# Performance work log

Hardware: AMD Instinct MI355X
Metric: run time of the kernel (lower is better)

Reference implementation:

```python
import jax, jax.numpy as jnp
import numpy as np

L = 2      # decoder layers
B = 4      # batch
T = 1000   # seq_len (mask built for this length)
C = 768    # input_dim / d_model
H = 12     # num_heads
DK = C // H
WIN = 100


def layernorm(x, g, b):
    m = x.mean(-1, keepdims=True)
    v = x.var(-1, keepdims=True)
    return (x - m) / jnp.sqrt(v + 1e-5) * g + b


def pos_encoding(t, c):
    # Transformer-XL / espnet RelPositionalEncoding table: relative positions t-1 .. -(t-1)
    rel = jnp.arange(t - 1, -t, -1, dtype=jnp.float32)          # (2t-1,)
    div = jnp.exp(-jnp.arange(0, c, 2, dtype=jnp.float32) * (np.log(10000.0) / c))
    ang = rel[:, None] * div[None, :]                            # (2t-1, c/2)
    pe = jnp.zeros((2 * t - 1, c), dtype=jnp.float32)
    pe = pe.at[:, 0::2].set(jnp.sin(ang)).at[:, 1::2].set(jnp.cos(ang))
    return pe


def rel_shift(x):
    # x: (B, H, T, 2T-1) -> (B, H, T, T), Transformer-XL relative shift
    b, h, t, p = x.shape
    xp = jnp.pad(x, ((0, 0), (0, 0), (0, 0), (1, 0)))
    xp = xp.reshape(b, h, p + 1, t)[:, :, 1:, :].reshape(b, h, t, p)
    return xp[..., :t]


def setup_inputs() -> dict:
    key = jax.random.key(0)
    ks = jax.random.split(key, 16)
    s = 0.02
    inp = {
        "x": jax.random.normal(ks[0], (B, T, C), dtype=jnp.float32),
        "Wq": jax.random.normal(ks[1], (L, C, C), dtype=jnp.float32) * s,
        "bq": jnp.zeros((L, C), dtype=jnp.float32),
        "Wk": jax.random.normal(ks[2], (L, C, C), dtype=jnp.float32) * s,
        "bk": jnp.zeros((L, C), dtype=jnp.float32),
        "Wv": jax.random.normal(ks[3], (L, C, C), dtype=jnp.float32) * s,
        "bv": jnp.zeros((L, C), dtype=jnp.float32),
        "Wo": jax.random.normal(ks[4], (L, C, C), dtype=jnp.float32) * s,
        "bo": jnp.zeros((L, C), dtype=jnp.float32),
        "Wp": jax.random.normal(ks[5], (L, C, C), dtype=jnp.float32) * s,   # linear_pos, no bias
        "pos_u": jax.random.normal(ks[6], (L, H, DK), dtype=jnp.float32) * s,
        "pos_v": jax.random.normal(ks[7], (L, H, DK), dtype=jnp.float32) * s,
        "ln1_g": jnp.ones((L, C), dtype=jnp.float32),
        "ln1_b": jnp.zeros((L, C), dtype=jnp.float32),
        "ln2_g": jnp.ones((L, C), dtype=jnp.float32),
        "ln2_b": jnp.zeros((L, C), dtype=jnp.float32),
        "W1": jax.random.normal(ks[8], (L, C, C), dtype=jnp.float32) * s,   # mlp_ratio = 1
        "b1": jnp.zeros((L, C), dtype=jnp.float32),
        "W2": jax.random.normal(ks[9], (L, C, C), dtype=jnp.float32) * s,
        "b2": jnp.zeros((L, C), dtype=jnp.float32),
    }
    # diagonal (banded) mask: True = blocked outside the attention window
    i = np.arange(T)
    blocked = np.abs(i[:, None] - i[None, :]) > (WIN // 2)
    inp["att_mask"] = jnp.asarray(blocked)
    return inp


def reference(x, att_mask, Wq, bq, Wk, bk, Wv, bv, Wo, bo, Wp, pos_u, pos_v,
              ln1_g, ln1_b, ln2_g, ln2_b, W1, b1, W2, b2):
    Bb, t, c = x.shape
    pe = pos_encoding(t, c)                       # (2T-1, C)
    h = x * jnp.sqrt(jnp.float32(c))              # xscale in RelPositionalEncoding
    for l in range(L):
        y = layernorm(h, ln1_g[l], ln1_b[l])
        q = (y @ Wq[l] + bq[l]).reshape(Bb, t, H, DK)
        k = (y @ Wk[l] + bk[l]).reshape(Bb, t, H, DK)
        v = (y @ Wv[l] + bv[l]).reshape(Bb, t, H, DK)
        p = (pe @ Wp[l]).reshape(2 * t - 1, H, DK)
        ac = jnp.einsum('bthd,bshd->bhts', q + pos_u[l], k)
        bd = rel_shift(jnp.einsum('bthd,phd->bhtp', q + pos_v[l], p))
        scores = (ac + bd) / jnp.sqrt(jnp.float32(DK))
        scores = jnp.where(att_mask[None, None], jnp.float32(-1e9), scores)
        attn = jax.nn.softmax(scores, axis=-1)
        o = jnp.einsum('bhts,bshd->bthd', attn, v).reshape(Bb, t, c)
        h = h + (o @ Wo[l] + bo[l])
        y2 = layernorm(h, ln2_g[l], ln2_b[l])
        h = h + (jax.nn.gelu(y2 @ W1[l] + b1[l]) @ W2[l] + b2[l])
    return h
```

## Files before the change

### kernel.cpp

```cpp
#include <hip/hip_runtime.h>
#include <math.h>

#define LNUM 2
#define BBATCH 4
#define TSEQ 1000
#define CDIM 768
#define HHEADS 12
#define DKK 64
#define PPOS (2*TSEQ-1)
#define HALFW 50
#define MROWS (BBATCH*TSEQ)
#define MPAD 4096
#define QKVDIM (3*CDIM)
#define NS 176

typedef __attribute__((ext_vector_type(8))) short s16x8;
typedef __attribute__((ext_vector_type(4))) short s16x4;
typedef __attribute__((ext_vector_type(4))) float f32x4;

#define LDSOFF(p) ((unsigned)(uintptr_t)(__attribute__((address_space(3))) const void*)(p))

__device__ __forceinline__ ushort f2bf(float x) {
    unsigned u = __float_as_uint(x);
    unsigned r = u + 0x7FFFu + ((u >> 16) & 1u);
    return (ushort)(r >> 16);
}
__device__ __forceinline__ float bf2f(ushort h) {
    return __uint_as_float(((unsigned)h) << 16);
}
__device__ __forceinline__ float gelu_f(float x) {
    float u = 0.7978845608028654f * (x + 0.044715f * x * x * x);
    return 0.5f * x * (1.f + tanhf(u));
}
__device__ __forceinline__ void gload_lds16(const void* g, void* l) {
    __builtin_amdgcn_global_load_lds(
        (const __attribute__((address_space(1))) void*)g,
        (__attribute__((address_space(3))) void*)l, 16, 0, 0);
}
__device__ __forceinline__ s16x4 tr_read(unsigned addr) {
    s16x4 d;
    asm volatile("ds_read_b64_tr_b16 %0, %1" : "=v"(d) : "v"(addr));
    return d;
}
__device__ __forceinline__ s16x4 tr_read128(unsigned addr) {
    s16x4 d;
    asm volatile("ds_read_b64_tr_b16 %0, %1 offset:128" : "=v"(d) : "v"(addr));
    return d;
}

__global__ __launch_bounds__(256) void transpose_pack(
    const float* __restrict__ Wq, const float* __restrict__ Wk,
    const float* __restrict__ Wv, const float* __restrict__ Wp,
    const float* __restrict__ Wo, const float* __restrict__ W1,
    const float* __restrict__ W2,
    ushort* __restrict__ Wtqkv, ushort* __restrict__ Wtp,
    ushort* __restrict__ Wto, ushort* __restrict__ Wt1, ushort* __restrict__ Wt2) {
    const int l = blockIdx.z / 7, m = blockIdx.z % 7;
    const float* srcs[7] = {Wq, Wk, Wv, Wp, Wo, W1, W2};
    const float* src = srcs[m] + (size_t)l * CDIM * CDIM;
    ushort* dst;
    if (m < 3)       dst = Wtqkv + (size_t)l * QKVDIM * CDIM + (size_t)m * CDIM * CDIM;
    else if (m == 3) dst = Wtp + (size_t)l * CDIM * CDIM;
    else if (m == 4) dst = Wto + (size_t)l * CDIM * CDIM;
    else if (m == 5) dst = Wt1 + (size_t)l * CDIM * CDIM;
    else             dst = Wt2 + (size_t)l * CDIM * CDIM;
    __shared__ float tile[32][33];
    const int tx = threadIdx.x, ty = threadIdx.y;
    const int c0 = blockIdx.x * 32, r0 = blockIdx.y * 32;
#pragma unroll
    for (int i = 0; i < 4; ++i)
        tile[ty + i * 8][tx] = src[(size_t)(r0 + ty + i * 8) * CDIM + c0 + tx];
    __syncthreads();
#pragma unroll
    for (int i = 0; i < 4; ++i)
        dst[(size_t)(c0 + ty + i * 8) * CDIM + r0 + tx] = f2bf(tile[tx][ty + i * 8]);
}

__global__ __launch_bounds__(256) void prep_small(ushort* __restrict__ pe,
                                                  const float* __restrict__ bq,
                                                  const float* __restrict__ bk,
                                                  const float* __restrict__ bv,
                                                  float* __restrict__ bqkv) {
    int idx = blockIdx.x * 256 + threadIdx.x;
    const int npair = 256 * (CDIM / 2);
    if (idx < npair) {
        int jloc = idx / (CDIM / 2);
        int m = idx - jloc * (CDIM / 2);
        int j = 896 + jloc;
        float rel = (float)(TSEQ - 1 - j);
        float div = expf(-(float)(2 * m) * (9.210340371976184f / (float)CDIM));
        float a = rel * div;
        pe[(size_t)j * CDIM + 2 * m]     = f2bf(sinf(a));
        pe[(size_t)j * CDIM + 2 * m + 1] = f2bf(cosf(a));
    }
    if (idx < LNUM * QKVDIM) {
        int l = idx / QKVDIM, c = idx - l * QKVDIM;
        float v;
        if (c < CDIM)            v = bq[l * CDIM + c];
        else if (c < 2 * CDIM)   v = bk[l * CDIM + c - CDIM];
        else                     v = bv[l * CDIM + c - 2 * CDIM];
        bqkv[idx] = v;
    }
}

__global__ __launch_bounds__(192) void ln_kernel(const float* __restrict__ in,
                                                 const float* __restrict__ g,
                                                 const float* __restrict__ bta,
                                                 ushort* __restrict__ y, float xscale) {
    const int row = blockIdx.x, tid = threadIdx.x;
    float4 v = *(const float4*)&in[(size_t)row * CDIM + tid * 4];
    v.x *= xscale; v.y *= xscale; v.z *= xscale; v.w *= xscale;
    float s  = v.x + v.y + v.z + v.w;
    float ss = v.x * v.x + v.y * v.y + v.z * v.z + v.w * v.w;
#pragma unroll
    for (int off = 32; off; off >>= 1) {
        s  += __shfl_xor(s, off);
        ss += __shfl_xor(ss, off);
    }
    __shared__ float sm[3], sq[3];
    const int wid = tid >> 6, lane = tid & 63;
    if (lane == 0) { sm[wid] = s; sq[wid] = ss; }
    __syncthreads();
    const float st  = sm[0] + sm[1] + sm[2];
    const float sst = sq[0] + sq[1] + sq[2];
    const float mean = st * (1.f / CDIM);
    const float var  = sst * (1.f / CDIM) - mean * mean;
    const float rstd = rsqrtf(var + 1e-5f);
    const float4 g4 = *(const float4*)&g[tid * 4];
    const float4 b4 = *(const float4*)&bta[tid * 4];
    ushort o0 = f2bf((v.x - mean) * rstd * g4.x + b4.x);
    ushort o1 = f2bf((v.y - mean) * rstd * g4.y + b4.y);
    ushort o2 = f2bf((v.z - mean) * rstd * g4.z + b4.z);
    ushort o3 = f2bf((v.w - mean) * rstd * g4.w + b4.w);
    uint2 pk; pk.x = (unsigned)o0 | ((unsigned)o1 << 16);
    pk.y = (unsigned)o2 | ((unsigned)o3 << 16);
    *(uint2*)&y[(size_t)row * CDIM + tid * 4] = pk;
}

template <int EPI>
__global__ __launch_bounds__(256, 3) void gemm64(const ushort* __restrict__ A,
                                                 const ushort* __restrict__ Bt,
                                                 const float* __restrict__ bias,
                                                 void* Out, int M, int ldo,
                                                 const float* resid, float rscale,
                                                 size_t zsB, size_t zsO) {
    __shared__ ushort lds[24576];
    const int tid = threadIdx.x;
    const int w = tid >> 6, lane = tid & 63;
    const int row0 = blockIdx.x * 64, col0 = blockIdx.y * 128;
    const size_t zb = blockIdx.z;
    Bt += zb * zsB;
    if (EPI == 2) Out = (void*)((float*)Out + zb * zsO);
    else          Out = (void*)((ushort*)Out + zb * zsO);

    const int srow8  = lane >> 3;
    const int schunk = (lane & 7) ^ srow8;

#define STAGE64(buf, k0)                                                        \
    {                                                                           \
        _Pragma("unroll")                                                       \
        for (int g = 0; g < 6; ++g) {                                           \
            const int grp = w * 6 + g;                                          \
            const int r = grp * 8 + srow8;                                      \
            const ushort* src = (grp < 8)                                       \
                ? A  + (size_t)(row0 + r) * CDIM + (k0) + schunk * 8            \
                : Bt + (size_t)(col0 + (r - 64)) * CDIM + (k0) + schunk * 8;    \
            gload_lds16(src, (char*)lds + (buf) * 24576 + grp * 1024);          \
        }                                                                       \
    }

    const int wm = (w >> 1) * 32, wn = (w & 1) * 64;
    const int lr = lane & 15, q = lane >> 4;
    f32x4 acc[2][4] = {};

    STAGE64(0, 0);
    __syncthreads();
    int cur = 0;
    for (int k0 = 0; k0 < CDIM; k0 += 64) {
        if (k0 + 64 < CDIM) STAGE64(cur ^ 1, k0 + 64);
        const int base = cur * 12288;
#pragma unroll
        for (int kk = 0; kk < 2; ++kk) {
            s16x8 af[2], bfr[4];
#pragma unroll
            for (int i = 0; i < 2; ++i) {
                const int r = wm + i * 16 + lr;
                af[i] = *(const s16x8*)&lds[base + r * 64 + ((((kk << 2) | q) ^ (r & 7)) << 3)];
            }
#pragma unroll
            for (int j = 0; j < 4; ++j) {
                const int r = 64 + wn + j * 16 + lr;
                bfr[j] = *(const s16x8*)&lds[base + r * 64 + ((((kk << 2) | q) ^ (r & 7)) << 3)];
            }
#pragma unroll
            for (int i = 0; i < 2; ++i)
#pragma unroll
                for (int j = 0; j < 4; ++j)
                    acc[i][j] = __builtin_amdgcn_mfma_f32_16x16x32_bf16(af[i], bfr[j], acc[i][j], 0, 0, 0);
        }
        __syncthreads();
        cur ^= 1;
    }
#undef STAGE64

    const int lrr = (lane >> 4) * 4;
    const int lc = lane & 15;
#pragma unroll
    for (int j = 0; j < 4; ++j) {
        const int col = col0 + wn + j * 16 + lc;
        const float bv = bias ? bias[col] : 0.f;
#pragma unroll
        for (int i = 0; i < 2; ++i) {
#pragma unroll
            for (int r = 0; r < 4; ++r) {
                const int row = row0 + wm + i * 16 + lrr + r;
                if (row >= M) continue;
                const float v = acc[i][j][r] + bv;
                if (EPI == 0)
                    ((ushort*)Out)[(size_t)row * ldo + col] = f2bf(v);
                else if (EPI == 1)
                    ((ushort*)Out)[(size_t)row * ldo + col] = f2bf(gelu_f(v));
                else {
                    float* p = (float*)Out + (size_t)row * ldo + col;
                    *p = resid[(size_t)row * ldo + col] * rscale + v;
                }
            }
        }
    }
}

__global__ __launch_bounds__(256, 3) void attn_mfma(
    const ushort* __restrict__ qkv, const ushort* __restrict__ pb,
    const float* __restrict__ pos_u, const float* __restrict__ pos_v,
    ushort* __restrict__ o) {
    __shared__ __align__(16) char smem[50176];
    ushort* Kl   = (ushort*)smem;
    ushort* Qraw = (ushort*)(smem + 25344);
    ushort* Bd   = (ushort*)(smem + 34560);
    ushort* Pl   = (ushort*)smem;
    ushort* Vsub = (ushort*)(smem + 25600);

    const int tid = threadIdx.x;
    const int w = tid >> 6, lane = tid & 63;
    const int t0 = blockIdx.x * 64;
    const int h = blockIdx.y, b = blockIdx.z;

    {
        const int row = tid >> 2, c = (tid & 3) << 4;
        int t = t0 + row; t = (t < TSEQ) ? t : TSEQ - 1;
        const ushort* qp = qkv + (size_t)(b * TSEQ + t) * QKVDIM + h * DKK + c;
        *(s16x8*)&Qraw[row * 72 + c]     = *(const s16x8*)qp;
        *(s16x8*)&Qraw[row * 72 + c + 8] = *(const s16x8*)(qp + 8);
    }
    for (int task = tid; task < NS * 4; task += 256) {
        const int j = task >> 2, c = (task & 3) << 4;
        int kb = t0 - HALFW + j; kb = kb < 0 ? 0 : (kb < TSEQ ? kb : TSEQ - 1);
        const ushort* kp = qkv + (size_t)(b * TSEQ + kb) * QKVDIM + CDIM + h * DKK + c;
        *(s16x8*)&Kl[j * 72 + c]     = *(const s16x8*)kp;
        *(s16x8*)&Kl[j * 72 + c + 8] = *(const s16x8*)(kp + 8);
    }
    __syncthreads();

    const int m0 = w * 16;
    const int lr = lane & 15, lk = (lane >> 4) * 8;
    const f32x4 zero = {0.f, 0.f, 0.f, 0.f};

    const ushort* pbh = pb + (size_t)949 * CDIM + h * DKK;
    s16x8 pfr[7][2];
#pragma unroll
    for (int uf = 0; uf < 7; ++uf) {
        pfr[uf][0] = *(const s16x8*)&pbh[(size_t)(uf * 16 + lr) * CDIM + lk];
        pfr[uf][1] = *(const s16x8*)&pbh[(size_t)(uf * 16 + lr) * CDIM + 32 + lk];
    }

    s16x8 qr0 = *(const s16x8*)&Qraw[(m0 + lr) * 72 + lk];
    s16x8 qr1 = *(const s16x8*)&Qraw[(m0 + lr) * 72 + 32 + lk];
    s16x8 qu0, qu1, qv0, qv1;
#pragma unroll
    for (int e = 0; e < 8; ++e) {
        const float q0 = bf2f((ushort)qr0[e]), q1 = bf2f((ushort)qr1[e]);
        qu0[e] = (short)f2bf(q0 + pos_u[h * DKK + lk + e]);
        qu1[e] = (short)f2bf(q1 + pos_u[h * DKK + 32 + lk + e]);
        qv0[e] = (short)f2bf(q0 + pos_v[h * DKK + lk + e]);
        qv1[e] = (short)f2bf(q1 + pos_v[h * DKK + 32 + lk + e]);
    }

    f32x4 acS[11], acB[7];
    __builtin_amdgcn_s_setprio(1);
#pragma unroll
    for (int uf = 0; uf < 7; ++uf) {
        acB[uf] = __builtin_amdgcn_mfma_f32_16x16x32_bf16(qv0, pfr[uf][0], zero, 0, 0, 0);
        acB[uf] = __builtin_amdgcn_mfma_f32_16x16x32_bf16(qv1, pfr[uf][1], acB[uf], 0, 0, 0);
    }
#pragma unroll
    for (int jf = 0; jf < 11; ++jf) {
        s16x8 k0 = *(const s16x8*)&Kl[(jf * 16 + lr) * 72 + lk];
        s16x8 k1 = *(const s16x8*)&Kl[(jf * 16 + lr) * 72 + 32 + lk];
        acS[jf] = __builtin_amdgcn_mfma_f32_16x16x32_bf16(qu0, k0, zero, 0, 0, 0);
        acS[jf] = __builtin_amdgcn_mfma_f32_16x16x32_bf16(qu1, k1, acS[jf], 0, 0, 0);
    }
    __builtin_amdgcn_s_setprio(0);

    ushort* bdw = Bd + w * 16 * 104;
#pragma unroll
    for (int uf = 0; uf < 7; ++uf)
#pragma unroll
        for (int r = 0; r < 4; ++r)
            bdw[((lane >> 4) * 4 + r) * 104 + uf * 16 + lr] = f2bf(acB[uf][r]);
    float mx[4] = {-1e30f, -1e30f, -1e30f, -1e30f};
#pragma unroll
    for (int jf = 0; jf < 11; ++jf)
#pragma unroll
        for (int r = 0; r < 4; ++r) {
            const int tl = (lane >> 4) * 4 + r;
            const int tloc = m0 + tl;
            const int j = jf * 16 + lr;
            const int u = j - tloc;
            const int s = t0 - HALFW + j;
            const bool valid = (u >= 0) & (u <= 2 * HALFW) & (s >= 0) & (s < TSEQ)
                               & (t0 + tloc < TSEQ);
            float sc = -1e30f;
            if (valid) sc = (acS[jf][r] + bf2f(bdw[tl * 104 + u])) * 0.125f;
            acS[jf][r] = sc;
            mx[r] = fmaxf(mx[r], sc);
        }
#pragma unroll
    for (int r = 0; r < 4; ++r)
#pragma unroll
        for (int off = 8; off; off >>= 1)
            mx[r] = fmaxf(mx[r], __shfl_xor(mx[r], off));
    float sm[4] = {0.f, 0.f, 0.f, 0.f};
#pragma unroll
    for (int jf = 0; jf < 11; ++jf)
#pragma unroll
        for (int r = 0; r < 4; ++r) {
            float e = __expf(acS[jf][r] - mx[r]);
            acS[jf][r] = e;
            sm[r] += e;
        }
#pragma unroll
    for (int r = 0; r < 4; ++r) {
#pragma unroll
        for (int off = 8; off; off >>= 1) sm[r] += __shfl_xor(sm[r], off);
        sm[r] = 1.f / sm[r];
    }
    __syncthreads();

#pragma unroll
    for (int jf = 0; jf < 11; ++jf)
#pragma unroll
        for (int r = 0; r < 4; ++r)
            Pl[(m0 + (lane >> 4) * 4 + r) * 200 + jf * 16 + lr] = f2bf(acS[jf][r]);
#pragma unroll
    for (int r = 0; r < 4; ++r)
        Pl[(m0 + (lane >> 4) * 4 + r) * 200 + 176 + lr] = 0;

    for (int sp = w; sp < 24; sp += 4) {
        const int ob = sp * 1024 + lane * 16;
        const int d0c = ob / 6144;
        const int rem = ob - d0c * 6144;
        const int j = rem >> 5;
        const int halfo = (rem & 31) >> 4;
        int t = t0 - HALFW + j; t = t < 0 ? 0 : (t < TSEQ ? t : TSEQ - 1);
        const ushort* src = qkv + (size_t)(b * TSEQ + t) * QKVDIM + 2 * CDIM
                            + h * DKK + d0c * 16 + halfo * 8;
        gload_lds16(src, (char*)Vsub + sp * 1024);
    }
    __syncthreads();

    s16x8 pa[6];
#pragma unroll
    for (int ks = 0; ks < 6; ++ks)
        pa[ks] = *(const s16x8*)&Pl[(m0 + lr) * 200 + ks * 32 + lk];
    const unsigned vbase = LDSOFF(Vsub);
    f32x4 acO[4] = {};
#pragma unroll
    for (int nf = 0; nf < 4; ++nf) {
        const unsigned abase = vbase + nf * 6144 + ((lane >> 4) << 8) + ((lane & 15) << 1);
        s16x4 lo[6], hi[6];
#pragma unroll
        for (int ks = 0; ks < 6; ++ks) {
            lo[ks] = tr_read(abase + ks * 1024);
            hi[ks] = tr_read128(abase + ks * 1024);
        }
        asm volatile("s_waitcnt lgkmcnt(0)" ::: "memory");
        __builtin_amdgcn_sched_barrier(0);
        __builtin_amdgcn_s_setprio(1);
#pragma unroll
        for (int ks = 0; ks < 6; ++ks) {
            s16x8 vb = __builtin_shufflevector(lo[ks], hi[ks], 0, 1, 2, 3, 4, 5, 6, 7);
            acO[nf] = __builtin_amdgcn_mfma_f32_16x16x32_bf16(pa[ks], vb, acO[nf], 0, 0, 0);
        }
        __builtin_amdgcn_s_setprio(0);
    }
#pragma unroll
    for (int nf = 0; nf < 4; ++nf)
#pragma unroll
        for (int r = 0; r < 4; ++r) {
            const int t = t0 + m0 + (lane >> 4) * 4 + r;
            if (t < TSEQ)
                o[(size_t)(b * TSEQ + t) * CDIM + h * DKK + nf * 16 + lr] =
                    f2bf(acO[nf][r] * sm[r]);
        }
}

extern "C" void kernel_launch(void* const* d_in, const int* in_sizes, int n_in,
                              void* d_out, int out_size, void* d_ws, size_t ws_size,
                              hipStream_t stream) {
    const float* x     = (const float*)d_in[0];
    const float* Wq    = (const float*)d_in[1];
    const float* bq    = (const float*)d_in[2];
    const float* Wk    = (const float*)d_in[3];
    const float* bk    = (const float*)d_in[4];
    const float* Wv    = (const float*)d_in[5];
    const float* bv    = (const float*)d_in[6];
    const float* Wo    = (const float*)d_in[7];
    const float* bo    = (const float*)d_in[8];
    const float* Wp    = (const float*)d_in[9];
    const float* pos_u = (const float*)d_in[10];
    const float* pos_v = (const float*)d_in[11];
    const float* ln1g  = (const float*)d_in[12];
    const float* ln1b  = (const float*)d_in[13];
    const float* ln2g  = (const float*)d_in[14];
    const float* ln2b  = (const float*)d_in[15];
    const float* W1    = (const float*)d_in[16];
    const float* b1    = (const float*)d_in[17];
    const float* W2    = (const float*)d_in[18];
    const float* b2    = (const float*)d_in[19];

    float* h = (float*)d_out;
    const float XS = 27.712812921102035f;

    char* p = (char*)d_ws;
    ushort* Wtqkv = (ushort*)p;               p += (size_t)LNUM * QKVDIM * CDIM * 2;
    ushort* Wtp   = (ushort*)p;               p += (size_t)LNUM * CDIM * CDIM * 2;
    ushort* Wto   = (ushort*)p;               p += (size_t)LNUM * CDIM * CDIM * 2;
    ushort* Wt1   = (ushort*)p;               p += (size_t)LNUM * CDIM * CDIM * 2;
    ushort* Wt2   = (ushort*)p;               p += (size_t)LNUM * CDIM * CDIM * 2;
    float*  bqkv  = (float*)p;                p += (size_t)LNUM * QKVDIM * 4;
    ushort* pe    = (ushort*)p;               p += (size_t)2048 * CDIM * 2;
    ushort* pb    = (ushort*)p;               p += (size_t)LNUM * 2048 * CDIM * 2;
    ushort* y     = (ushort*)p;               p += (size_t)MPAD * CDIM * 2;
    ushort* qkv   = (ushort*)p;               p += (size_t)MPAD * QKVDIM * 2;
    ushort* o     = (ushort*)p;               p += (size_t)MPAD * CDIM * 2;
    ushort* hid   = (ushort*)p;               p += (size_t)MPAD * CDIM * 2;

    transpose_pack<<<dim3(24, 24, LNUM * 7), dim3(32, 8), 0, stream>>>(
        Wq, Wk, Wv, Wp, Wo, W1, W2, Wtqkv, Wtp, Wto, Wt1, Wt2);
    prep_small<<<384, 256, 0, stream>>>(pe, bq, bk, bv, bqkv);

    const int MB = (MROWS + 63) / 64;
    const dim3 gQKV(MB, QKVDIM / 128);
    const dim3 gC(MB, CDIM / 128);
    const dim3 gP(4, CDIM / 128, LNUM);
    const dim3 gA(16, HHEADS, BBATCH);

    gemm64<0><<<gP, 256, 0, stream>>>(pe + (size_t)896 * CDIM, Wtp, nullptr,
                                      pb + (size_t)896 * CDIM, 256, CDIM,
                                      nullptr, 0.f,
                                      (size_t)CDIM * CDIM, (size_t)2048 * CDIM);

    for (int l = 0; l < LNUM; ++l) {
        const size_t wo = (size_t)l * CDIM * CDIM;
        const float* res1 = (l == 0) ? x : h;
        const float rs1   = (l == 0) ? XS : 1.f;
        ln_kernel<<<MROWS, 192, 0, stream>>>(res1, ln1g + l * CDIM, ln1b + l * CDIM, y, rs1);
        gemm64<0><<<gQKV, 256, 0, stream>>>(y, Wtqkv + (size_t)l * QKVDIM * CDIM,
                                            bqkv + l * QKVDIM, qkv, MROWS, QKVDIM,
                                            nullptr, 0.f, 0, 0);
        attn_mfma<<<gA, 256, 0, stream>>>(
            qkv, pb + (size_t)l * 2048 * CDIM,
            pos_u + l * HHEADS * DKK, pos_v + l * HHEADS * DKK, o);
        gemm64<2><<<gC, 256, 0, stream>>>(o, Wto + wo, bo + l * CDIM, h, MROWS, CDIM,
                                          res1, rs1, 0, 0);
        ln_kernel<<<MROWS, 192, 0, stream>>>(h, ln2g + l * CDIM, ln2b + l * CDIM, y, 1.f);
        gemm64<1><<<gC, 256, 0, stream>>>(y, Wt1 + wo, b1 + l * CDIM, hid, MROWS, CDIM,
                                          nullptr, 0.f, 0, 0);
        gemm64<2><<<gC, 256, 0, stream>>>(hid, Wt2 + wo, b2 + l * CDIM, h, MROWS, CDIM,
                                          h, 1.f, 0, 0);
    }
}
```

Baseline: 262.0 us.

## Prefetch V and K asynchronously into LDS and split PV into two halves

```diff
diff --git a/kernel.cpp b/kernel.cpp
--- a/kernel.cpp
+++ b/kernel.cpp
@@ -233,37 +233,45 @@
     const ushort* __restrict__ qkv, const ushort* __restrict__ pb,
     const float* __restrict__ pos_u, const float* __restrict__ pos_v,
     ushort* __restrict__ o) {
-    __shared__ __align__(16) char smem[50176];
+    __shared__ __align__(16) char smem[51200];
     ushort* Kl   = (ushort*)smem;
-    ushort* Qraw = (ushort*)(smem + 25344);
-    ushort* Bd   = (ushort*)(smem + 34560);
     ushort* Pl   = (ushort*)smem;
     ushort* Vsub = (ushort*)(smem + 25600);
+    ushort* Bd   = (ushort*)(smem + 37888);
 
     const int tid = threadIdx.x;
     const int w = tid >> 6, lane = tid & 63;
     const int t0 = blockIdx.x * 64;
     const int h = blockIdx.y, b = blockIdx.z;
-
-    {
-        const int row = tid >> 2, c = (tid & 3) << 4;
-        int t = t0 + row; t = (t < TSEQ) ? t : TSEQ - 1;
-        const ushort* qp = qkv + (size_t)(b * TSEQ + t) * QKVDIM + h * DKK + c;
-        *(s16x8*)&Qraw[row * 72 + c]     = *(const s16x8*)qp;
-        *(s16x8*)&Qraw[row * 72 + c + 8] = *(const s16x8*)(qp + 8);
-    }
-    for (int task = tid; task < NS * 4; task += 256) {
-        const int j = task >> 2, c = (task & 3) << 4;
-        int kb = t0 - HALFW + j; kb = kb < 0 ? 0 : (kb < TSEQ ? kb : TSEQ - 1);
-        const ushort* kp = qkv + (size_t)(b * TSEQ + kb) * QKVDIM + CDIM + h * DKK + c;
-        *(s16x8*)&Kl[j * 72 + c]     = *(const s16x8*)kp;
-        *(s16x8*)&Kl[j * 72 + c + 8] = *(const s16x8*)(kp + 8);
-    }
-    __syncthreads();
-
     const int m0 = w * 16;
-    const int lr = lane & 15, lk = (lane >> 4) * 8;
-    const f32x4 zero = {0.f, 0.f, 0.f, 0.f};
+    const int lr = lane & 15, lk = (lane >> 4) * 8, q = lane >> 4;
+
+    auto vsrc = [&](int sp) -> const ushort* {
+        const int ob = sp * 1024 + lane * 16;
+        const int d0c = ob / 6144;
+        const int rem = ob - d0c * 6144;
+        const int j = rem >> 5;
+        const int halfo = (rem & 31) >> 4;
+        int t = t0 - HALFW + j; t = t < 0 ? 0 : (t < TSEQ ? t : TSEQ - 1);
+        return qkv + (size_t)(b * TSEQ + t) * QKVDIM + 2 * CDIM + h * DKK
+               + (d0c & 1) * 16 + halfo * 8;
+    };
+
+    int tq = t0 + m0 + lr; tq = tq < TSEQ ? tq : TSEQ - 1;
+    const ushort* qp = qkv + (size_t)(b * TSEQ + tq) * QKVDIM + h * DKK;
+    s16x8 qr0 = *(const s16x8*)(qp + lk);
+    s16x8 qr1 = *(const s16x8*)(qp + 32 + lk);
+    const float* puB = pos_u + h * DKK;
+    const float* pvB = pos_v + h * DKK;
+    float puA[16], pvA[16];
+    *(float4*)&puA[0]  = *(const float4*)(puB + lk);
+    *(float4*)&puA[4]  = *(const float4*)(puB + lk + 4);
+    *(float4*)&puA[8]  = *(const float4*)(puB + 32 + lk);
+    *(float4*)&puA[12] = *(const float4*)(puB + 32 + lk + 4);
+    *(float4*)&pvA[0]  = *(const float4*)(pvB + lk);
+    *(float4*)&pvA[4]  = *(const float4*)(pvB + lk + 4);
+    *(float4*)&pvA[8]  = *(const float4*)(pvB + 32 + lk);
+    *(float4*)&pvA[12] = *(const float4*)(pvB + 32 + lk + 4);
 
     const ushort* pbh = pb + (size_t)949 * CDIM + h * DKK;
     s16x8 pfr[7][2];
@@ -273,18 +281,40 @@
         pfr[uf][1] = *(const s16x8*)&pbh[(size_t)(uf * 16 + lr) * CDIM + 32 + lk];
     }
 
-    s16x8 qr0 = *(const s16x8*)&Qraw[(m0 + lr) * 72 + lk];
-    s16x8 qr1 = *(const s16x8*)&Qraw[(m0 + lr) * 72 + 32 + lk];
+#pragma unroll
+    for (int g = 0; g < 3; ++g) {
+        const int sp = w * 3 + g;
+        gload_lds16(vsrc(sp), (char*)Vsub + sp * 1024);
+    }
+
+    {
+        const int srow8 = lane >> 3;
+        const int schunk = (lane & 7) ^ srow8;
+#pragma unroll
+        for (int g = 0; g < 6; ++g) {
+            const int sp = w * 6 + g;
+            if (sp < 22) {
+                const int r = sp * 8 + srow8;
+                int kb = t0 - HALFW + r; kb = kb < 0 ? 0 : (kb < TSEQ ? kb : TSEQ - 1);
+                const ushort* src = qkv + (size_t)(b * TSEQ + kb) * QKVDIM + CDIM
+                                    + h * DKK + schunk * 8;
+                gload_lds16(src, (char*)Kl + sp * 1024);
+            }
+        }
+    }
+
     s16x8 qu0, qu1, qv0, qv1;
 #pragma unroll
     for (int e = 0; e < 8; ++e) {
         const float q0 = bf2f((ushort)qr0[e]), q1 = bf2f((ushort)qr1[e]);
-        qu0[e] = (short)f2bf(q0 + pos_u[h * DKK + lk + e]);
-        qu1[e] = (short)f2bf(q1 + pos_u[h * DKK + 32 + lk + e]);
-        qv0[e] = (short)f2bf(q0 + pos_v[h * DKK + lk + e]);
-        qv1[e] = (short)f2bf(q1 + pos_v[h * DKK + 32 + lk + e]);
-    }
-
+        qu0[e] = (short)f2bf(q0 + puA[e]);
+        qu1[e] = (short)f2bf(q1 + puA[8 + e]);
+        qv0[e] = (short)f2bf(q0 + pvA[e]);
+        qv1[e] = (short)f2bf(q1 + pvA[8 + e]);
+    }
+    __syncthreads();
+
+    const f32x4 zero = {0.f, 0.f, 0.f, 0.f};
     f32x4 acS[11], acB[7];
     __builtin_amdgcn_s_setprio(1);
 #pragma unroll
@@ -294,8 +324,10 @@
     }
 #pragma unroll
     for (int jf = 0; jf < 11; ++jf) {
-        s16x8 k0 = *(const s16x8*)&Kl[(jf * 16 + lr) * 72 + lk];
-        s16x8 k1 = *(const s16x8*)&Kl[(jf * 16 + lr) * 72 + 32 + lk];
+        const int rr = jf * 16 + lr;
+        const int sw = rr & 7;
+        s16x8 k0 = *(const s16x8*)&Kl[rr * 64 + (((q)     ^ sw) << 3)];
+        s16x8 k1 = *(const s16x8*)&Kl[rr * 64 + (((q | 4) ^ sw) << 3)];
         acS[jf] = __builtin_amdgcn_mfma_f32_16x16x32_bf16(qu0, k0, zero, 0, 0, 0);
         acS[jf] = __builtin_amdgcn_mfma_f32_16x16x32_bf16(qu1, k1, acS[jf], 0, 0, 0);
     }
@@ -346,6 +378,10 @@
     }
     __syncthreads();
 
+    s16x8 vr0 = *vsrc(12 + w * 3 + 0);
+    s16x8 vr1 = *vsrc(12 + w * 3 + 1);
+    s16x8 vr2 = *vsrc(12 + w * 3 + 2);
+
 #pragma unroll
     for (int jf = 0; jf < 11; ++jf)
 #pragma unroll
@@ -355,28 +391,15 @@
     for (int r = 0; r < 4; ++r)
         Pl[(m0 + (lane >> 4) * 4 + r) * 200 + 176 + lr] = 0;
 
-    for (int sp = w; sp < 24; sp += 4) {
-        const int ob = sp * 1024 + lane * 16;
-        const int d0c = ob / 6144;
-        const int rem = ob - d0c * 6144;
-        const int j = rem >> 5;
-        const int halfo = (rem & 31) >> 4;
-        int t = t0 - HALFW + j; t = t < 0 ? 0 : (t < TSEQ ? t : TSEQ - 1);
-        const ushort* src = qkv + (size_t)(b * TSEQ + t) * QKVDIM + 2 * CDIM
-                            + h * DKK + d0c * 16 + halfo * 8;
-        gload_lds16(src, (char*)Vsub + sp * 1024);
-    }
-    __syncthreads();
-
     s16x8 pa[6];
 #pragma unroll
     for (int ks = 0; ks < 6; ++ks)
         pa[ks] = *(const s16x8*)&Pl[(m0 + lr) * 200 + ks * 32 + lk];
+
     const unsigned vbase = LDSOFF(Vsub);
-    f32x4 acO[4] = {};
-#pragma unroll
-    for (int nf = 0; nf < 4; ++nf) {
-        const unsigned abase = vbase + nf * 6144 + ((lane >> 4) << 8) + ((lane & 15) << 1);
+#pragma unroll
+    for (int nf = 0; nf < 2; ++nf) {
+        const unsigned abase = vbase + (nf & 1) * 6144 + ((lane >> 4) << 8) + ((lane & 15) << 1);
         s16x4 lo[6], hi[6];
 #pragma unroll
         for (int ks = 0; ks < 6; ++ks) {
@@ -385,23 +408,56 @@
         }
         asm volatile("s_waitcnt lgkmcnt(0)" ::: "memory");
         __builtin_amdgcn_sched_barrier(0);
+        f32x4 acO = {};
         __builtin_amdgcn_s_setprio(1);
 #pragma unroll
         for (int ks = 0; ks < 6; ++ks) {
             s16x8 vb = __builtin_shufflevector(lo[ks], hi[ks], 0, 1, 2, 3, 4, 5, 6, 7);
-            acO[nf] = __builtin_amdgcn_mfma_f32_16x16x32_bf16(pa[ks], vb, acO[nf], 0, 0, 0);
+            acO = __builtin_amdgcn_mfma_f32_16x16x32_bf16(pa[ks], vb, acO, 0, 0, 0);
         }
         __builtin_amdgcn_s_setprio(0);
-    }
-#pragma unroll
-    for (int nf = 0; nf < 4; ++nf)
 #pragma unroll
         for (int r = 0; r < 4; ++r) {
             const int t = t0 + m0 + (lane >> 4) * 4 + r;
             if (t < TSEQ)
                 o[(size_t)(b * TSEQ + t) * CDIM + h * DKK + nf * 16 + lr] =
-                    f2bf(acO[nf][r] * sm[r]);
-        }
+                    f2bf(acO[r] * sm[r]);
+        }
+    }
+    __syncthreads();
+
+    *(s16x8*)((char*)Vsub + (w * 3 + 0) * 1024 + lane * 16) = vr0;
+    *(s16x8*)((char*)Vsub + (w * 3 + 1) * 1024 + lane * 16) = vr1;
+    *(s16x8*)((char*)Vsub + (w * 3 + 2) * 1024 + lane * 16) = vr2;
+    __syncthreads();
+
+#pragma unroll
+    for (int nf = 2; nf < 4; ++nf) {
+        const unsigned abase = vbase + (nf & 1) * 6144 + ((lane >> 4) << 8) + ((lane & 15) << 1);
+        s16x4 lo[6], hi[6];
+#pragma unroll
+        for (int ks = 0; ks < 6; ++ks) {
+            lo[ks] = tr_read(abase + ks * 1024);
+            hi[ks] = tr_read128(abase + ks * 1024);
+        }
+        asm volatile("s_waitcnt lgkmcnt(0)" ::: "memory");
+        __builtin_amdgcn_sched_barrier(0);
+        f32x4 acO = {};
+        __builtin_amdgcn_s_setprio(1);
+#pragma unroll
+        for (int ks = 0; ks < 6; ++ks) {
+            s16x8 vb = __builtin_shufflevector(lo[ks], hi[ks], 0, 1, 2, 3, 4, 5, 6, 7);
+            acO = __builtin_amdgcn_mfma_f32_16x16x32_bf16(pa[ks], vb, acO, 0, 0, 0);
+        }
+        __builtin_amdgcn_s_setprio(0);
+#pragma unroll
+        for (int r = 0; r < 4; ++r) {
+            const int t = t0 + m0 + (lane >> 4) * 4 + r;
+            if (t < TSEQ)
+                o[(size_t)(b * TSEQ + t) * CDIM + h * DKK + nf * 16 + lr] =
+                    f2bf(acO[r] * sm[r]);
+        }
+    }
 }
 
 extern "C" void kernel_launch(void* const* d_in, const int* in_sizes, int n_in,
```

New measurement: 261.5 us. Within noise of the previous version (-0.2%).
